# Optimization experiments

Hardware: AMD Instinct MI355X
Metric: run time of the kernel (lower is better)

The kernel has to match this reference:

```python
import jax, jax.numpy as jnp
import numpy as np

B, F, V, E = 65536, 39, 100000, 16
EPS = 1e-5

def setup_inputs() -> dict:
    key = jax.random.key(0)
    ks = jax.random.split(key, 10)
    return {
        'Xi': jax.random.randint(ks[0], (B, F, 1), 0, V, dtype=jnp.int64) if jax.config.read('jax_enable_x64') else jax.random.randint(ks[0], (B, F, 1), 0, V, dtype=jnp.int32),
        'Xv': jax.random.uniform(ks[1], (B, F), dtype=jnp.float32),
        'emb1': jax.random.normal(ks[2], (F, V, 1), dtype=jnp.float32),
        'emb2': jax.random.normal(ks[3], (F, V, E), dtype=jnp.float32),
        'W1': jax.random.normal(ks[4], (F * E, 512), dtype=jnp.float32) * 0.02,
        'b1': jax.random.normal(ks[5], (512,), dtype=jnp.float32) * 0.02,
        'g1': jnp.ones((512,), jnp.float32),
        'be1': jnp.zeros((512,), jnp.float32),
        'W2': jax.random.normal(ks[6], (512, 256), dtype=jnp.float32) * 0.02,
        'b2': jax.random.normal(ks[7], (256,), dtype=jnp.float32) * 0.02,
        'g2': jnp.ones((256,), jnp.float32),
        'be2': jnp.zeros((256,), jnp.float32),
        'bias': jax.random.normal(ks[8], (1,), dtype=jnp.float32),
    }

def _batchnorm(x, g, b):
    mu = jnp.mean(x, axis=0)
    var = jnp.mean(jnp.square(x - mu), axis=0)  # biased var, torch BN training mode
    return (x - mu) * jax.lax.rsqrt(var + EPS) * g + b

def reference(Xi, Xv, emb1, emb2, W1, b1, g1, be1, W2, b2, g2, be2, bias):
    idx = Xi[:, :, 0]                                # [B, F]
    fidx = jnp.arange(F)[None, :]                    # [1, F]
    # fused per-field gathers: [B, F] and [B, F, E]
    first = emb1[fidx, idx, 0] * Xv                  # first-order, [B, F]
    fm2 = emb2[fidx, idx] * Xv[:, :, None]           # second-order embeds, [B, F, E]
    sum_emb = jnp.sum(fm2, axis=1)                   # [B, E]
    second = 0.5 * (jnp.square(sum_emb) - jnp.sum(jnp.square(fm2), axis=1))  # [B, E]
    # deep part (note: original forward never applies the final num_classes layer)
    deep = fm2.reshape(B, F * E)
    deep = _batchnorm(deep @ W1 + b1, g1, be1)
    deep = _batchnorm(deep @ W2 + b2, g2, be2)
    return bias + jnp.sum(first, axis=1) + jnp.sum(second, axis=1) + jnp.sum(deep, axis=1)
```

## Files before the change

kernel.cpp:

```cpp
#include <hip/hip_runtime.h>

#define B_ROWS 65536
#define F_FEAT 39
#define V_VOC  100000
#define D_PAD  640
#define BN_EPS 1e-5f

typedef __bf16 bf16x8 __attribute__((ext_vector_type(8)));
typedef float  f32x16 __attribute__((ext_vector_type(16)));

__device__ __forceinline__ unsigned short toBF(float x) {
  unsigned int u = __float_as_uint(x);
  u += 0x7fffu + ((u >> 16) & 1u);
  return (unsigned short)(u >> 16);
}

__global__ __launch_bounds__(256) void k1_gather(
    const int* __restrict__ Xi, const float* __restrict__ Xv,
    const float* __restrict__ emb2, unsigned short* __restrict__ XT,
    float* __restrict__ fs, float* __restrict__ Mz) {
  if (threadIdx.x < 200)
    Mz[(size_t)blockIdx.x * 200 + threadIdx.x] = 0.f;

  const int b0 = blockIdx.x * 32;
  __shared__ int            sIdx[32][40];
  __shared__ float          sXv[32][40];
  __shared__ unsigned short xt[32][648];

  for (int u = threadIdx.x; u < 32 * 39; u += 256) {
    int r = u / 39, f = u - r * 39;
    sIdx[r][f] = Xi[(size_t)(b0 + r) * 39 + f];
    sXv[r][f]  = Xv[(size_t)(b0 + r) * 39 + f];
  }
  __syncthreads();

  const int r = threadIdx.x >> 3, ec = threadIdx.x & 7;
  float sv0 = 0.f, sv1 = 0.f, ss0 = 0.f, ss1 = 0.f;
#pragma unroll 4
  for (int f = 0; f < 39; ++f) {
    int id = sIdx[r][f];
    float xv = sXv[r][f];
    const float2 v = *reinterpret_cast<const float2*>(
        emb2 + ((size_t)f * V_VOC + id) * 16 + ec * 2);
    float a = v.x * xv, b = v.y * xv;
    sv0 += a; ss0 += a * a;
    sv1 += b; ss1 += b * b;
    unsigned int pk = (unsigned int)toBF(a) | ((unsigned int)toBF(b) << 16);
    *reinterpret_cast<unsigned int*>(&xt[r][f * 16 + ec * 2]) = pk;
  }
  float p = (sv0 * sv0 - ss0) + (sv1 * sv1 - ss1);
  p += __shfl_xor(p, 1);
  p += __shfl_xor(p, 2);
  p += __shfl_xor(p, 4);
  if (ec == 0) fs[b0 + r] = 0.5f * p;
  __syncthreads();

  for (int m = threadIdx.x; m < 640; m += 256) {
    unsigned short* dst = XT + (size_t)m * B_ROWS + b0;
    unsigned int q[16];
    if (m < 624) {
#pragma unroll
      for (int rr = 0; rr < 16; ++rr)
        q[rr] = (unsigned int)xt[2 * rr][m] | ((unsigned int)xt[2 * rr + 1][m] << 16);
    } else {
      unsigned int fill = (m == 624) ? 0x3f803f80u : 0u;
#pragma unroll
      for (int rr = 0; rr < 16; ++rr) q[rr] = fill;
    }
#pragma unroll
    for (int c = 0; c < 4; ++c) {
      uint4 w;
      w.x = q[c * 4]; w.y = q[c * 4 + 1]; w.z = q[c * 4 + 2]; w.w = q[c * 4 + 3];
      *reinterpret_cast<uint4*>(dst + c * 8) = w;
    }
  }
}

#define KSPLIT 32
__global__ __launch_bounds__(256) void k2_syrk(const unsigned short* __restrict__ XT,
                                               float* __restrict__ M) {
  const int ks = blockIdx.x & (KSPLIT - 1);
  int pair = blockIdx.x >> 5;
  int ti = 0, p = pair;
  while (p >= 5 - ti) { p -= 5 - ti; ++ti; }
  const int tj = ti + p;

  __shared__ unsigned short pa[128 * 64];
  __shared__ unsigned short pb[128 * 64];

  const int lane = threadIdx.x & 63, wid = threadIdx.x >> 6;
  const int wm = wid >> 1, wn = wid & 1;
  const int rl = lane & 31, hh = lane >> 5;

  f32x16 acc00, acc01, acc10, acc11;
#pragma unroll
  for (int i = 0; i < 16; ++i) { acc00[i] = 0.f; acc01[i] = 0.f; acc10[i] = 0.f; acc11[i] = 0.f; }

  const int krange = B_ROWS / KSPLIT;
  const int kbase = ks * krange;

  for (int kt = 0; kt < krange; kt += 64) {
    const int k0 = kbase + kt;
#pragma unroll
    for (int g2 = 0; g2 < 4; ++g2) {
      const int g = threadIdx.x + g2 * 256;
      const int r = g >> 3, j = g & 7;
      uint4 va = *reinterpret_cast<const uint4*>(XT + (size_t)(ti * 128 + r) * B_ROWS + k0 + j * 8);
      *reinterpret_cast<uint4*>((char*)pa + r * 128 + ((j ^ (r & 7)) << 4)) = va;
      uint4 vb = *reinterpret_cast<const uint4*>(XT + (size_t)(tj * 128 + r) * B_ROWS + k0 + j * 8);
      *reinterpret_cast<uint4*>((char*)pb + r * 128 + ((j ^ (r & 7)) << 4)) = vb;
    }
    __syncthreads();
#pragma unroll
    for (int kc = 0; kc < 4; ++kc) {
      const int ra0 = wm * 64 + rl, ra1 = wm * 64 + 32 + rl;
      const int rb0 = wn * 64 + rl, rb1 = wn * 64 + 32 + rl;
      bf16x8 a0 = *reinterpret_cast<const bf16x8*>((char*)pa + ra0 * 128 + (((kc * 2 + hh) ^ (ra0 & 7)) << 4));
      bf16x8 a1 = *reinterpret_cast<const bf16x8*>((char*)pa + ra1 * 128 + (((kc * 2 + hh) ^ (ra1 & 7)) << 4));
      bf16x8 b0 = *reinterpret_cast<const bf16x8*>((char*)pb + rb0 * 128 + (((kc * 2 + hh) ^ (rb0 & 7)) << 4));
      bf16x8 b1 = *reinterpret_cast<const bf16x8*>((char*)pb + rb1 * 128 + (((kc * 2 + hh) ^ (rb1 & 7)) << 4));
      acc00 = __builtin_amdgcn_mfma_f32_32x32x16_bf16(a0, b0, acc00, 0, 0, 0);
      acc01 = __builtin_amdgcn_mfma_f32_32x32x16_bf16(a0, b1, acc01, 0, 0, 0);
      acc10 = __builtin_amdgcn_mfma_f32_32x32x16_bf16(a1, b0, acc10, 0, 0, 0);
      acc11 = __builtin_amdgcn_mfma_f32_32x32x16_bf16(a1, b1, acc11, 0, 0, 0);
    }
    __syncthreads();
  }

#pragma unroll
  for (int rr = 0; rr < 16; ++rr) {
    const int rloc = (rr & 3) + ((rr >> 2) << 3) + hh * 4;
    const int row0 = ti * 128 + wm * 64 + rloc;
    const int row1 = row0 + 32;
    const int col0 = tj * 128 + wn * 64 + rl;
    atomicAdd(&M[row0 * D_PAD + col0], acc00[rr]);
    atomicAdd(&M[row0 * D_PAD + col0 + 32], acc01[rr]);
    atomicAdd(&M[row1 * D_PAD + col0], acc10[rr]);
    atomicAdd(&M[row1 * D_PAD + col0 + 32], acc11[rr]);
  }
}

__device__ __forceinline__ float fetchM(const float* M, int a, int b) {
  if ((a >> 7) > (b >> 7)) { int t = a; a = b; b = t; }
  return M[a * D_PAD + b];
}
__global__ void k3a_cov(const float* __restrict__ M, float* __restrict__ Cov,
                        float* __restrict__ mu) {
  const int i = blockIdx.x;
  const float inv = 1.f / 65536.f;
  const float mui = fetchM(M, 624, i) * inv;
  for (int j = threadIdx.x; j < D_PAD; j += 256) {
    float muj = fetchM(M, 624, j) * inv;
    Cov[i * D_PAD + j] = fetchM(M, i, j) * inv - mui * muj;
    if (i == 0) mu[j] = muj;
  }
}

__global__ __launch_bounds__(256) void qform(const float* __restrict__ Cov,
                                             const float* __restrict__ W, const int ldw,
                                             const float* __restrict__ g,
                                             float* __restrict__ alpha) {
  const int k0 = blockIdx.x * 2;
  __shared__ float w0s[624], w1s[624];
  for (int i = threadIdx.x; i < 624; i += 256) {
    w0s[i] = W[(size_t)i * ldw + k0];
    w1s[i] = W[(size_t)i * ldw + k0 + 1];
  }
  __syncthreads();
  const int j0 = threadIdx.x, j1 = threadIdx.x + 256, j2 = threadIdx.x + 512;
  const bool v2 = (j2 < 624);
  const float wj00 = w0s[j0], wj01 = w0s[j1], wj02 = v2 ? w0s[j2] : 0.f;
  const float wj10 = w1s[j0], wj11 = w1s[j1], wj12 = v2 ? w1s[j2] : 0.f;
  float acc0 = 0.f, acc1 = 0.f;
  for (int i = 0; i < 624; ++i) {
    const float wi0 = w0s[i], wi1 = w1s[i];
    const float* row = Cov + i * D_PAD;
    const float c0 = row[j0], c1 = row[j1], c2 = v2 ? row[j2] : 0.f;
    acc0 += wi0 * (c0 * wj00 + c1 * wj01 + c2 * wj02);
    acc1 += wi1 * (c0 * wj10 + c1 * wj11 + c2 * wj12);
  }
#pragma unroll
  for (int off = 32; off > 0; off >>= 1) {
    acc0 += __shfl_down(acc0, off);
    acc1 += __shfl_down(acc1, off);
  }
  __shared__ float pr[2][4];
  const int lane = threadIdx.x & 63, wv = threadIdx.x >> 6;
  if (lane == 0) { pr[0][wv] = acc0; pr[1][wv] = acc1; }
  __syncthreads();
  if (threadIdx.x == 0) {
    float v0 = pr[0][0] + pr[0][1] + pr[0][2] + pr[0][3];
    float v1 = pr[1][0] + pr[1][1] + pr[1][2] + pr[1][3];
    alpha[k0]     = g[k0]     * rsqrtf(v0 + BN_EPS);
    alpha[k0 + 1] = g[k0 + 1] * rsqrtf(v1 + BN_EPS);
  }
}

__global__ __launch_bounds__(256) void k3c_G(const float* __restrict__ W1,
                                             const float* __restrict__ alpha1,
                                             const float* __restrict__ W2,
                                             float* __restrict__ G) {
  const int i = blockIdx.x;
  __shared__ float a[512];
  for (int k = threadIdx.x; k < 512; k += 256)
    a[k] = W1[(size_t)i * 512 + k] * alpha1[k];
  __syncthreads();
  const int j = threadIdx.x;
  float acc = 0.f;
#pragma unroll 8
  for (int k = 0; k < 512; ++k) acc += a[k] * W2[(size_t)k * 256 + j];
  G[(size_t)i * 256 + j] = acc;
}

__global__ __launch_bounds__(256) void k3e_final(const float* __restrict__ G,
                                                 const float* __restrict__ alpha2,
                                                 const float* __restrict__ mu,
                                                 const float* __restrict__ be2,
                                                 const float* __restrict__ bias,
                                                 float* __restrict__ gw,
                                                 float* __restrict__ consts) {
  __shared__ float a2[256];
  __shared__ float gws[640];
  a2[threadIdx.x] = alpha2[threadIdx.x];
  __syncthreads();
  for (int i = threadIdx.x; i < 640; i += 256) {
    float acc = 0.f;
    if (i < 624) {
      const float* gr = G + (size_t)i * 256;
#pragma unroll 8
      for (int j = 0; j < 256; ++j) acc += gr[j] * a2[j];
    }
    gw[i] = acc;
    gws[i] = acc;
  }
  __syncthreads();
  float pm = 0.f;
  for (int i = threadIdx.x; i < 624; i += 256) pm += mu[i] * gws[i];
  float val = be2[threadIdx.x] - pm;
#pragma unroll
  for (int off = 32; off > 0; off >>= 1) val += __shfl_down(val, off);
  __shared__ float pr[4];
  const int lane = threadIdx.x & 63, wv = threadIdx.x >> 6;
  if (lane == 0) pr[wv] = val;
  __syncthreads();
  if (threadIdx.x == 0) consts[0] = bias[0] + pr[0] + pr[1] + pr[2] + pr[3];
}

__global__ __launch_bounds__(256) void k4_table(const float* __restrict__ emb1,
                                                const float* __restrict__ emb2,
                                                const float* __restrict__ gw,
                                                float* __restrict__ tp) {
  const int f = blockIdx.y;
  const int v = blockIdx.x * 256 + threadIdx.x;
  __shared__ float gf[16];
  if (threadIdx.x < 16) gf[threadIdx.x] = gw[f * 16 + threadIdx.x];
  __syncthreads();
  if (v >= V_VOC) return;
  const float* e = emb2 + ((size_t)f * V_VOC + v) * 16;
  float4 x0 = *reinterpret_cast<const float4*>(e);
  float4 x1 = *reinterpret_cast<const float4*>(e + 4);
  float4 x2 = *reinterpret_cast<const float4*>(e + 8);
  float4 x3 = *reinterpret_cast<const float4*>(e + 12);
  float d = x0.x * gf[0] + x0.y * gf[1] + x0.z * gf[2] + x0.w * gf[3]
          + x1.x * gf[4] + x1.y * gf[5] + x1.z * gf[6] + x1.w * gf[7]
          + x2.x * gf[8] + x2.y * gf[9] + x2.z * gf[10] + x2.w * gf[11]
          + x3.x * gf[12] + x3.y * gf[13] + x3.z * gf[14] + x3.w * gf[15];
  tp[(size_t)f * V_VOC + v] = emb1[(size_t)f * V_VOC + v] + d;
}

__global__ __launch_bounds__(256) void k5_out(const int* __restrict__ Xi,
                                              const float* __restrict__ Xv,
                                              const float* __restrict__ tp,
                                              const float* __restrict__ fs,
                                              const float* __restrict__ consts,
                                              float* __restrict__ out) {
  const int b0 = blockIdx.x * 128;
  __shared__ int   si[128 * 39];
  __shared__ float sx[128 * 39];
  for (int u = threadIdx.x; u < 128 * 39; u += 256) {
    si[u] = Xi[(size_t)b0 * 39 + u];
    sx[u] = Xv[(size_t)b0 * 39 + u];
  }
  __syncthreads();
  const int r = threadIdx.x >> 1, hf = threadIdx.x & 1;
  const int fb = hf ? 20 : 0, fe = hf ? 39 : 20;
  float acc = 0.f;
  for (int f = fb; f < fe; ++f) {
    int id = si[r * 39 + f];
    acc += sx[r * 39 + f] * tp[f * V_VOC + id];
  }
  acc += __shfl_xor(acc, 1);
  if (hf == 0) out[b0 + r] = acc + fs[b0 + r] + consts[0];
}

extern "C" void kernel_launch(void* const* d_in, const int* in_sizes, int n_in,
                              void* d_out, int out_size, void* d_ws, size_t ws_size,
                              hipStream_t stream) {
  const int*   Xi   = (const int*)d_in[0];
  const float* Xv   = (const float*)d_in[1];
  const float* emb1 = (const float*)d_in[2];
  const float* emb2 = (const float*)d_in[3];
  const float* W1   = (const float*)d_in[4];
  const float* g1   = (const float*)d_in[6];
  const float* W2   = (const float*)d_in[8];
  const float* g2   = (const float*)d_in[10];
  const float* be2  = (const float*)d_in[11];
  const float* bias = (const float*)d_in[12];
  float* out = (float*)d_out;
  char* ws = (char*)d_ws;

  const size_t OFF_XT  = 0;
  const size_t OFF_M   = OFF_XT + (size_t)640 * 65536 * 2;
  const size_t OFF_COV = OFF_M + (size_t)640 * 640 * 4;
  const size_t OFF_MU  = OFF_COV + (size_t)640 * 640 * 4;
  const size_t OFF_A1  = OFF_MU + 640 * 4;
  const size_t OFF_A2  = OFF_A1 + 512 * 4;
  const size_t OFF_G   = OFF_A2 + 256 * 4;
  const size_t OFF_GW  = OFF_G + (size_t)624 * 256 * 4;
  const size_t OFF_CN  = OFF_GW + 640 * 4;
  const size_t OFF_FS  = OFF_CN + 256;
  const size_t OFF_TP  = OFF_FS + (size_t)65536 * 4;

  unsigned short* XT = (unsigned short*)(ws + OFF_XT);
  float* M   = (float*)(ws + OFF_M);
  float* COV = (float*)(ws + OFF_COV);
  float* MU  = (float*)(ws + OFF_MU);
  float* A1  = (float*)(ws + OFF_A1);
  float* A2  = (float*)(ws + OFF_A2);
  float* G   = (float*)(ws + OFF_G);
  float* GW  = (float*)(ws + OFF_GW);
  float* CN  = (float*)(ws + OFF_CN);
  float* FS  = (float*)(ws + OFF_FS);
  float* TP  = (float*)(ws + OFF_TP);

  k1_gather<<<2048, 256, 0, stream>>>(Xi, Xv, emb2, XT, FS, M);
  k2_syrk<<<15 * KSPLIT, 256, 0, stream>>>(XT, M);
  k3a_cov<<<640, 256, 0, stream>>>(M, COV, MU);
  qform<<<256, 256, 0, stream>>>(COV, W1, 512, g1, A1);
  k3c_G<<<624, 256, 0, stream>>>(W1, A1, W2, G);
  qform<<<128, 256, 0, stream>>>(COV, G, 256, g2, A2);
  k3e_final<<<1, 256, 0, stream>>>(G, A2, MU, be2, bias, GW, CN);
  k4_table<<<dim3(391, 39), 256, 0, stream>>>(emb1, emb2, GW, TP);
  k5_out<<<512, 256, 0, stream>>>(Xi, Xv, TP, FS, CN, out);
}
```

Before: 377.1 us.

## Replace full-vocab projection table with per-row dot over gathered bf16 embeddings

The first-order term is now gathered inside the gather kernel and folded into the per-row partial sum. The k4 pass, which read the entire emb2 table (about 250MB) to build a projected lookup table, is removed. In its place, a k5_dot kernel computes each row's deep contribution as a dot product of the already-materialized bf16 XT columns with gw. This drops a large full-table sweep at the cost of re-reading XT (about 80MB) and using bf16-rounded embeddings for the deep dot, which adds rounding error.

```diff
diff --git a/kernel.cpp b/kernel.cpp
--- a/kernel.cpp
+++ b/kernel.cpp
@@ -17,8 +17,9 @@
 
 __global__ __launch_bounds__(256) void k1_gather(
     const int* __restrict__ Xi, const float* __restrict__ Xv,
-    const float* __restrict__ emb2, unsigned short* __restrict__ XT,
-    float* __restrict__ fs, float* __restrict__ Mz) {
+    const float* __restrict__ emb1, const float* __restrict__ emb2,
+    unsigned short* __restrict__ XT, float* __restrict__ fs,
+    float* __restrict__ Mz) {
   if (threadIdx.x < 200)
     Mz[(size_t)blockIdx.x * 200 + threadIdx.x] = 0.f;
 
@@ -48,29 +49,33 @@
     unsigned int pk = (unsigned int)toBF(a) | ((unsigned int)toBF(b) << 16);
     *reinterpret_cast<unsigned int*>(&xt[r][f * 16 + ec * 2]) = pk;
   }
-  float p = (sv0 * sv0 - ss0) + (sv1 * sv1 - ss1);
-  p += __shfl_xor(p, 1);
-  p += __shfl_xor(p, 2);
-  p += __shfl_xor(p, 4);
-  if (ec == 0) fs[b0 + r] = 0.5f * p;
+  float fo = 0.f;
+  for (int f = ec; f < 39; f += 8)
+    fo += emb1[(size_t)f * V_VOC + sIdx[r][f]] * sXv[r][f];
+
+  float q = 0.5f * ((sv0 * sv0 - ss0) + (sv1 * sv1 - ss1)) + fo;
+  q += __shfl_xor(q, 1);
+  q += __shfl_xor(q, 2);
+  q += __shfl_xor(q, 4);
+  if (ec == 0) fs[b0 + r] = q;
   __syncthreads();
 
   for (int m = threadIdx.x; m < 640; m += 256) {
     unsigned short* dst = XT + (size_t)m * B_ROWS + b0;
-    unsigned int q[16];
+    unsigned int q2[16];
     if (m < 624) {
 #pragma unroll
       for (int rr = 0; rr < 16; ++rr)
-        q[rr] = (unsigned int)xt[2 * rr][m] | ((unsigned int)xt[2 * rr + 1][m] << 16);
+        q2[rr] = (unsigned int)xt[2 * rr][m] | ((unsigned int)xt[2 * rr + 1][m] << 16);
     } else {
       unsigned int fill = (m == 624) ? 0x3f803f80u : 0u;
 #pragma unroll
-      for (int rr = 0; rr < 16; ++rr) q[rr] = fill;
+      for (int rr = 0; rr < 16; ++rr) q2[rr] = fill;
     }
 #pragma unroll
     for (int c = 0; c < 4; ++c) {
       uint4 w;
-      w.x = q[c * 4]; w.y = q[c * 4 + 1]; w.z = q[c * 4 + 2]; w.w = q[c * 4 + 3];
+      w.x = q2[c * 4]; w.y = q2[c * 4 + 1]; w.z = q2[c * 4 + 2]; w.w = q2[c * 4 + 3];
       *reinterpret_cast<uint4*>(dst + c * 8) = w;
     }
   }
@@ -246,51 +251,23 @@
   if (threadIdx.x == 0) consts[0] = bias[0] + pr[0] + pr[1] + pr[2] + pr[3];
 }
 
-__global__ __launch_bounds__(256) void k4_table(const float* __restrict__ emb1,
-                                                const float* __restrict__ emb2,
-                                                const float* __restrict__ gw,
-                                                float* __restrict__ tp) {
-  const int f = blockIdx.y;
-  const int v = blockIdx.x * 256 + threadIdx.x;
-  __shared__ float gf[16];
-  if (threadIdx.x < 16) gf[threadIdx.x] = gw[f * 16 + threadIdx.x];
-  __syncthreads();
-  if (v >= V_VOC) return;
-  const float* e = emb2 + ((size_t)f * V_VOC + v) * 16;
-  float4 x0 = *reinterpret_cast<const float4*>(e);
-  float4 x1 = *reinterpret_cast<const float4*>(e + 4);
-  float4 x2 = *reinterpret_cast<const float4*>(e + 8);
-  float4 x3 = *reinterpret_cast<const float4*>(e + 12);
-  float d = x0.x * gf[0] + x0.y * gf[1] + x0.z * gf[2] + x0.w * gf[3]
-          + x1.x * gf[4] + x1.y * gf[5] + x1.z * gf[6] + x1.w * gf[7]
-          + x2.x * gf[8] + x2.y * gf[9] + x2.z * gf[10] + x2.w * gf[11]
-          + x3.x * gf[12] + x3.y * gf[13] + x3.z * gf[14] + x3.w * gf[15];
-  tp[(size_t)f * V_VOC + v] = emb1[(size_t)f * V_VOC + v] + d;
-}
-
-__global__ __launch_bounds__(256) void k5_out(const int* __restrict__ Xi,
-                                              const float* __restrict__ Xv,
-                                              const float* __restrict__ tp,
+__global__ __launch_bounds__(256) void k5_dot(const unsigned short* __restrict__ XT,
+                                              const float* __restrict__ gw,
                                               const float* __restrict__ fs,
                                               const float* __restrict__ consts,
                                               float* __restrict__ out) {
-  const int b0 = blockIdx.x * 128;
-  __shared__ int   si[128 * 39];
-  __shared__ float sx[128 * 39];
-  for (int u = threadIdx.x; u < 128 * 39; u += 256) {
-    si[u] = Xi[(size_t)b0 * 39 + u];
-    sx[u] = Xv[(size_t)b0 * 39 + u];
-  }
-  __syncthreads();
-  const int r = threadIdx.x >> 1, hf = threadIdx.x & 1;
-  const int fb = hf ? 20 : 0, fe = hf ? 39 : 20;
+  __shared__ float g[624];
+  for (int m = threadIdx.x; m < 624; m += 256) g[m] = gw[m];
+  __syncthreads();
+  const int b = blockIdx.x * 256 + threadIdx.x;
+  const unsigned short* col = XT + b;
   float acc = 0.f;
-  for (int f = fb; f < fe; ++f) {
-    int id = si[r * 39 + f];
-    acc += sx[r * 39 + f] * tp[f * V_VOC + id];
-  }
-  acc += __shfl_xor(acc, 1);
-  if (hf == 0) out[b0 + r] = acc + fs[b0 + r] + consts[0];
+#pragma unroll 8
+  for (int m = 0; m < 624; ++m) {
+    unsigned int u = (unsigned int)col[(size_t)m * B_ROWS] << 16;
+    acc += __uint_as_float(u) * g[m];
+  }
+  out[b] = acc + fs[b] + consts[0];
 }
 
 extern "C" void kernel_launch(void* const* d_in, const int* in_sizes, int n_in,
@@ -319,7 +296,6 @@
   const size_t OFF_GW  = OFF_G + (size_t)624 * 256 * 4;
   const size_t OFF_CN  = OFF_GW + 640 * 4;
   const size_t OFF_FS  = OFF_CN + 256;
-  const size_t OFF_TP  = OFF_FS + (size_t)65536 * 4;
 
   unsigned short* XT = (unsigned short*)(ws + OFF_XT);
   float* M   = (float*)(ws + OFF_M);
@@ -331,15 +307,13 @@
   float* GW  = (float*)(ws + OFF_GW);
   float* CN  = (float*)(ws + OFF_CN);
   float* FS  = (float*)(ws + OFF_FS);
-  float* TP  = (float*)(ws + OFF_TP);
-
-  k1_gather<<<2048, 256, 0, stream>>>(Xi, Xv, emb2, XT, FS, M);
+
+  k1_gather<<<2048, 256, 0, stream>>>(Xi, Xv, emb1, emb2, XT, FS, M);
   k2_syrk<<<15 * KSPLIT, 256, 0, stream>>>(XT, M);
   k3a_cov<<<640, 256, 0, stream>>>(M, COV, MU);
   qform<<<256, 256, 0, stream>>>(COV, W1, 512, g1, A1);
   k3c_G<<<624, 256, 0, stream>>>(W1, A1, W2, G);
   qform<<<128, 256, 0, stream>>>(COV, G, 256, g2, A2);
   k3e_final<<<1, 256, 0, stream>>>(G, A2, MU, be2, bias, GW, CN);
-  k4_table<<<dim3(391, 39), 256, 0, stream>>>(emb1, emb2, GW, TP);
-  k5_out<<<512, 256, 0, stream>>>(Xi, Xv, TP, FS, CN, out);
-}
+  k5_dot<<<256, 256, 0, stream>>>(XT, GW, FS, CN, out);
+}
```

After: 384.0 us. No clear change (+1.8%).
